# Optimization experiments

Measured on AMD Instinct MI355X. Metric: run time of the kernel, lower is better.

The kernel has to match this reference:

```python
import jax, jax.numpy as jnp
import numpy as np

DIM = 128; D_STATE = 16; D_CONV = 4; EXPAND = 2
D_INNER = DIM * EXPAND            # 256
DT_RANK = (DIM + 15) // 16        # 8
B, H, W = 2, 56, 56


def _ln(x, w, b):
    m = jnp.mean(x, -1, keepdims=True)
    v = jnp.var(x, -1, keepdims=True)
    return (x - m) * jax.lax.rsqrt(v + 1e-5) * w + b


def _mamba(x, in_w, conv_w, conv_b, xproj_w, dt_w, dt_b, A_log, Dp, out_w):
    # x: (B, L, DIM)
    Bb, L, _ = x.shape
    xz = x @ in_w.T                                   # (B,L,2*D_INNER)
    xi, z = jnp.split(xz, 2, axis=-1)
    # causal depthwise conv1d (pad left d_conv-1, truncate to L)
    xc = jnp.transpose(xi, (0, 2, 1))                 # (B,D_INNER,L)
    xc = jax.lax.conv_general_dilated(
        xc, conv_w, (1,), [(D_CONV - 1, 0)],
        dimension_numbers=('NCH', 'OIH', 'NCH'),
        feature_group_count=D_INNER) + conv_b[None, :, None]
    xs = jax.nn.silu(jnp.transpose(xc, (0, 2, 1)))    # (B,L,D_INNER)
    dbl = xs @ xproj_w.T                              # (B,L,DT_RANK+2*D_STATE)
    dt = jax.nn.softplus(dbl[..., :DT_RANK] @ dt_w.T + dt_b)   # (B,L,D_INNER)
    Bc = dbl[..., DT_RANK:DT_RANK + D_STATE]          # (B,L,D_STATE)
    Cc = dbl[..., DT_RANK + D_STATE:]                 # (B,L,D_STATE)
    A = -jnp.exp(A_log)                               # (D_INNER,D_STATE)
    dA = jnp.exp(dt[..., None] * A)                   # (B,L,D_INNER,D_STATE)
    dBu = (dt * xs)[..., None] * Bc[:, :, None, :]    # (B,L,D_INNER,D_STATE)

    def step(h, inp):
        a, bu, c = inp
        h = a * h + bu                                # (B,D_INNER,D_STATE)
        return h, jnp.einsum('bdn,bn->bd', h, c)

    h0 = jnp.zeros((Bb, D_INNER, D_STATE), x.dtype)
    _, ys = jax.lax.scan(step, h0, (jnp.moveaxis(dA, 1, 0),
                                    jnp.moveaxis(dBu, 1, 0),
                                    jnp.moveaxis(Cc, 1, 0)))
    y = jnp.moveaxis(ys, 0, 1) + xs * Dp              # (B,L,D_INNER)
    y = y * jax.nn.silu(z)
    return y @ out_w.T                                # (B,L,DIM)


def _forward(x, norm_h_w, norm_h_b, norm_v_w, norm_v_b,
             dw_w, dw_b, pw_w, pw_b,
             h_in_w, h_conv_w, h_conv_b, h_xproj_w, h_dt_w, h_dt_b, h_A_log, h_D, h_out_w,
             v_in_w, v_conv_w, v_conv_b, v_xproj_w, v_dt_w, v_dt_b, v_A_log, v_D, v_out_w,
             ca_fc1_w, ca_fc2_w):
    Bb, C, Hh, Ww = x.shape
    # local branch: depthwise 3x3 + GELU + 1x1
    lf = jax.lax.conv_general_dilated(
        x, dw_w, (1, 1), [(1, 1), (1, 1)],
        dimension_numbers=('NCHW', 'OIHW', 'NCHW'),
        feature_group_count=C) + dw_b[None, :, None, None]
    lf = jax.nn.gelu(lf, approximate=False)
    lf = jnp.einsum('bchw,oc->bohw', lf, pw_w[:, :, 0, 0]) + pw_b[None, :, None, None]
    # horizontal scan: row-major tokens
    xh = _ln(x.reshape(Bb, C, Hh * Ww).transpose(0, 2, 1), norm_h_w, norm_h_b)
    oh = _mamba(xh, h_in_w, h_conv_w, h_conv_b, h_xproj_w, h_dt_w, h_dt_b,
                h_A_log, h_D, h_out_w)
    oh = oh.transpose(0, 2, 1).reshape(Bb, C, Hh, Ww)
    # vertical scan: column-major tokens
    xv = _ln(jnp.transpose(x, (0, 1, 3, 2)).reshape(Bb, C, Ww * Hh).transpose(0, 2, 1),
             norm_v_w, norm_v_b)
    ov = _mamba(xv, v_in_w, v_conv_w, v_conv_b, v_xproj_w, v_dt_w, v_dt_b,
                v_A_log, v_D, v_out_w)
    ov = jnp.transpose(ov.transpose(0, 2, 1).reshape(Bb, C, Ww, Hh), (0, 1, 3, 2))
    fused = oh + ov + lf
    # channel attention
    y = jnp.mean(fused, axis=(2, 3))                  # (B,C)
    y = jax.nn.sigmoid(jax.nn.relu(y @ ca_fc1_w.T) @ ca_fc2_w.T)
    return fused * y[:, :, None, None] + x


def setup_inputs() -> dict:
    key = jax.random.key(0)
    ks = iter(jax.random.split(key, 64))
    def nrm(shape, scale):
        return jax.random.normal(next(ks), shape, jnp.float32) * scale
    d = {}
    d['x'] = nrm((B, DIM, H, W), 1.0)
    d['norm_h_w'] = jnp.ones((DIM,), jnp.float32); d['norm_h_b'] = jnp.zeros((DIM,), jnp.float32)
    d['norm_v_w'] = jnp.ones((DIM,), jnp.float32); d['norm_v_b'] = jnp.zeros((DIM,), jnp.float32)
    d['dw_w'] = nrm((DIM, 1, 3, 3), 1.0 / 3.0)
    d['dw_b'] = jnp.zeros((DIM,), jnp.float32)
    d['pw_w'] = nrm((DIM, DIM, 1, 1), DIM ** -0.5)
    d['pw_b'] = jnp.zeros((DIM,), jnp.float32)
    for p in ('h', 'v'):
        d[p + '_in_w'] = nrm((2 * D_INNER, DIM), DIM ** -0.5)
        d[p + '_conv_w'] = nrm((D_INNER, 1, D_CONV), D_CONV ** -0.5)
        d[p + '_conv_b'] = jnp.zeros((D_INNER,), jnp.float32)
        d[p + '_xproj_w'] = nrm((DT_RANK + 2 * D_STATE, D_INNER), D_INNER ** -0.5)
        d[p + '_dt_w'] = nrm((D_INNER, DT_RANK), DT_RANK ** -0.5)
        d[p + '_dt_b'] = jnp.full((D_INNER,), -2.0, jnp.float32)  # small positive dt
        d[p + '_A_log'] = jnp.log(jnp.tile(jnp.arange(1, D_STATE + 1, dtype=jnp.float32), (D_INNER, 1)))
        d[p + '_D'] = jnp.ones((D_INNER,), jnp.float32)
        d[p + '_out_w'] = nrm((DIM, D_INNER), D_INNER ** -0.5)
    d['ca_fc1_w'] = nrm((DIM // 4, DIM), DIM ** -0.5)
    d['ca_fc2_w'] = nrm((DIM, DIM // 4), (DIM // 4) ** -0.5)
    return d


def reference(x, norm_h_w, norm_h_b, norm_v_w, norm_v_b,
              dw_w, dw_b, pw_w, pw_b,
              h_in_w, h_conv_w, h_conv_b, h_xproj_w, h_dt_w, h_dt_b, h_A_log, h_D, h_out_w,
              v_in_w, v_conv_w, v_conv_b, v_xproj_w, v_dt_w, v_dt_b, v_A_log, v_D, v_out_w,
              ca_fc1_w, ca_fc2_w):
    return _forward(x, norm_h_w, norm_h_b, norm_v_w, norm_v_b,
                    dw_w, dw_b, pw_w, pw_b,
                    h_in_w, h_conv_w, h_conv_b, h_xproj_w, h_dt_w, h_dt_b, h_A_log, h_D, h_out_w,
                    v_in_w, v_conv_w, v_conv_b, v_xproj_w, v_dt_w, v_dt_b, v_A_log, v_D, v_out_w,
                    ca_fc1_w, ca_fc2_w)
```

## Files before the change

### kernel.cpp

```cpp
#include <hip/hip_runtime.h>
#include <hip/hip_bf16.h>

typedef __hip_bfloat16 bf16;
__device__ __forceinline__ float b2f(bf16 v){ return __bfloat162float(v); }
__device__ __forceinline__ bf16 f2b(float v){ return __float2bfloat16(v); }

typedef __attribute__((ext_vector_type(8))) short frag_ab;
typedef __attribute__((ext_vector_type(4))) float frag_cd;
typedef __attribute__((ext_vector_type(4))) short short4v;

__device__ __forceinline__ frag_ab ld_frag_2xb64(const bf16* p){
  union { frag_ab f; short4v h[2]; } u;
  u.h[0] = *reinterpret_cast<const short4v*>(p);
  u.h[1] = *reinterpret_cast<const short4v*>(p+4);
  return u.f;
}

#define LLEN 3136
#define BATCH 2
#define NCHUNK 49
#define LC 64

__global__ void k_front(const float* __restrict__ x, const float* __restrict__ dww,
                        const float* __restrict__ dwb, bf16* __restrict__ tmp,
                        const float* nhw_, const float* nhb_, const float* nvw_,
                        const float* nvb_, bf16* __restrict__ xln,
                        const float* __restrict__ h_inw, const float* __restrict__ v_inw,
                        const float* __restrict__ h_ow,  const float* __restrict__ v_ow,
                        const float* __restrict__ pww,   const float* __restrict__ h_xw,
                        const float* __restrict__ v_xw,
                        bf16* __restrict__ WBIN, bf16* __restrict__ WBOUT,
                        bf16* __restrict__ WBPW, bf16* __restrict__ WBX,
                        float* __restrict__ TSUMP){
  int blk = blockIdx.x;
  int tid = threadIdx.x;
  if (blk < 1024){
    int bc = blk & 255;
    int seg = blk >> 8;
    int c = bc & 127;
    const float* xp = x + (size_t)bc*LLEN;
    __shared__ float sxr[16][60];
    __shared__ float wsum[4];
    int r0 = seg*14;
    for (int idx = tid; idx < 16*56; idx += 256){
      int rr = idx/56, cc = idx%56;
      int gr = r0 - 1 + rr;
      sxr[rr][cc+1] = (gr >= 0 && gr < 56) ? xp[gr*56+cc] : 0.f;
    }
    if (tid < 16){ sxr[tid][0] = 0.f; sxr[tid][57] = 0.f; }
    float w[9];
    #pragma unroll
    for (int i=0;i<9;i++) w[i] = dww[c*9+i];
    float bias = dwb[c];
    __syncthreads();
    int pstart = seg * 784;
    float ts = 0.f;
    for (int p = pstart + tid; p < pstart + 784; p += 256){
      int i = p/56, j = p%56;
      int li = i - r0;
      float acc = bias;
      #pragma unroll
      for (int a=0;a<3;a++)
        #pragma unroll
        for (int bb=0;bb<3;bb++)
          acc += w[a*3+bb] * sxr[li+a][j+bb];
      float g = 0.5f*acc*(1.0f + erff(acc*0.70710678118654752f));
      bf16 gb = f2b(g);
      tmp[(size_t)bc*LLEN + p] = gb;
      ts += b2f(gb);
    }
    ts += __shfl_xor(ts, 1, 64);
    ts += __shfl_xor(ts, 2, 64);
    ts += __shfl_xor(ts, 4, 64);
    ts += __shfl_xor(ts, 8, 64);
    ts += __shfl_xor(ts, 16, 64);
    ts += __shfl_xor(ts, 32, 64);
    if ((tid & 63) == 0) wsum[tid >> 6] = ts;
    __syncthreads();
    if (tid == 0) TSUMP[seg*256 + bc] = wsum[0]+wsum[1]+wsum[2]+wsum[3];
  } else if (blk < 1136){
    int idx2 = blk - 1024;
    int h = idx2 % 56, b = idx2 / 56;
    __shared__ float sx[128][57];
    __shared__ float smean[56], srstd[56];
    __shared__ float wh[128], bh[128], wv_[128], bv_[128];
    if (tid < 128){ wh[tid]=nhw_[tid]; bh[tid]=nhb_[tid];
                    wv_[tid]=nvw_[tid]; bv_[tid]=nvb_[tid]; }
    for (int idx = tid; idx < 128*56; idx += 256){
      int c = idx / 56, w = idx % 56;
      sx[c][w] = x[((size_t)(b*128+c))*LLEN + h*56 + w];
    }
    __syncthreads();
    if (tid < 56){
      float s=0.f, s2=0.f;
      for (int c=0;c<128;c++){ float v = sx[c][tid]; s+=v; s2+=v*v; }
      float m = s*(1.f/128.f);
      float var = s2*(1.f/128.f) - m*m;
      smean[tid]=m; srstd[tid]=rsqrtf(var+1e-5f);
    }
    __syncthreads();
    bf16* outh = xln;
    bf16* outv = xln + (size_t)BATCH*LLEN*128;
    for (int idx = tid; idx < 56*128; idx += 256){
      int w = idx >> 7, c = idx & 127;
      float v = (sx[c][w]-smean[w])*srstd[w];
      outh[((size_t)b*LLEN + h*56 + w)*128 + c] = f2b(v*wh[c]+bh[c]);
      outv[((size_t)b*LLEN + w*56 + h)*128 + c] = f2b(v*wv_[c]+bv_[c]);
    }
  } else {
    int pblk = blk - 1136;
    int t16 = tid*16;
    if (pblk < 32){
      int g = pblk*4096 + t16;
      int dir = g >> 16, off = g & 65535;
      const float* src = (dir ? v_inw : h_inw) + off;
      bf16* dst = WBIN + g;
      #pragma unroll
      for (int r=0;r<4;r++){
        float4 w4 = *reinterpret_cast<const float4*>(src + r*4);
        bf16 t4[4] = {f2b(w4.x), f2b(w4.y), f2b(w4.z), f2b(w4.w)};
        *reinterpret_cast<double*>(dst + r*4) = *reinterpret_cast<double*>(t4);
      }
    } else if (pblk < 48){
      int g = (pblk-32)*4096 + t16;
      int dir = g >> 15, off = g & 32767;
      const float* src = (dir ? v_ow : h_ow) + off;
      bf16* dst = WBOUT + g;
      #pragma unroll
      for (int r=0;r<4;r++){
        float4 w4 = *reinterpret_cast<const float4*>(src + r*4);
        bf16 t4[4] = {f2b(w4.x), f2b(w4.y), f2b(w4.z), f2b(w4.w)};
        *reinterpret_cast<double*>(dst + r*4) = *reinterpret_cast<double*>(t4);
      }
    } else if (pblk < 52){
      int g = (pblk-48)*4096 + t16;
      const float* src = pww + g;
      bf16* dst = WBPW + g;
      #pragma unroll
      for (int r=0;r<4;r++){
        float4 w4 = *reinterpret_cast<const float4*>(src + r*4);
        bf16 t4[4] = {f2b(w4.x), f2b(w4.y), f2b(w4.z), f2b(w4.w)};
        *reinterpret_cast<double*>(dst + r*4) = *reinterpret_cast<double*>(t4);
      }
    } else if (pblk < 58){
      int g = (pblk-52)*4096 + t16;
      int dir = (g >= 12288) ? 1 : 0;
      int off = g - dir*12288;
      int rr = off >> 8, cc = off & 255;
      bf16* dst = WBX + g;
      if (rr < 40){
        const float* src = (dir ? v_xw : h_xw) + rr*256 + cc;
        #pragma unroll
        for (int r=0;r<4;r++){
          float4 w4 = *reinterpret_cast<const float4*>(src + r*4);
          bf16 t4[4] = {f2b(w4.x), f2b(w4.y), f2b(w4.z), f2b(w4.w)};
          *reinterpret_cast<double*>(dst + r*4) = *reinterpret_cast<double*>(t4);
        }
      } else {
        bf16 z4[4] = {f2b(0.f), f2b(0.f), f2b(0.f), f2b(0.f)};
        double zd = *reinterpret_cast<double*>(z4);
        #pragma unroll
        for (int r=0;r<4;r++) *reinterpret_cast<double*>(dst + r*4) = zd;
      }
    }
  }
}

__global__ void k_inproj(const bf16* __restrict__ xln, const bf16* __restrict__ WBIN,
                         bf16* __restrict__ XI, bf16* __restrict__ Z){
  int dir = blockIdx.z;
  const bf16* A = xln + (size_t)dir*BATCH*LLEN*128;
  const bf16* Wb = WBIN + (size_t)dir*512*128;
  int m0 = blockIdx.x*64;
  int npair = blockIdx.y*128;
  __shared__ __align__(16) bf16 sA[64][136];
  __shared__ __align__(16) bf16 sW[64][136];
  int tid = threadIdx.x;
  #pragma unroll
  for (int r=0;r<4;r++){
    int idx = tid + r*256;
    int row = idx >> 4, c8 = (idx & 15)*8;
    *reinterpret_cast<float4*>(&sA[row][c8]) =
        *reinterpret_cast<const float4*>(&A[(size_t)(m0+row)*128 + c8]);
  }
  int wv2 = tid >> 6, lane = tid & 63;
  int qd = lane >> 4, mr = lane & 15;
  bf16* dst = (npair < 256) ? XI : Z;
  int nbase0 = npair & 255;
  size_t dslab = (size_t)dir*BATCH*LLEN*256;
  #pragma unroll
  for (int nt=0; nt<2; nt++){
    int n0 = npair + nt*64;
    __syncthreads();
    #pragma unroll
    for (int r=0;r<4;r++){
      int idx = tid + r*256;
      int row = idx >> 4, c8 = (idx & 15)*8;
      *reinterpret_cast<float4*>(&sW[row][c8]) =
          *reinterpret_cast<const float4*>(&Wb[(size_t)(n0+row)*128 + c8]);
    }
    __syncthreads();
    frag_cd acc[4] = {};
    #pragma unroll
    for (int k0=0;k0<128;k0+=32){
      frag_ab af = *reinterpret_cast<frag_ab*>(&sA[wv2*16+mr][k0+qd*8]);
      #pragma unroll
      for (int t=0;t<4;t++){
        frag_ab bfr = *reinterpret_cast<frag_ab*>(&sW[t*16+mr][k0+qd*8]);
        acc[t] = __builtin_amdgcn_mfma_f32_16x16x32_bf16(af, bfr, acc[t], 0, 0, 0);
      }
    }
    int nb = nbase0 + nt*64;
    #pragma unroll
    for (int t=0;t<4;t++)
      #pragma unroll
      for (int r=0;r<4;r++){
        int row = m0 + wv2*16 + qd*4 + r;
        int col = nb + t*16 + mr;
        dst[dslab + (size_t)row*256 + col] = f2b(acc[t][r]);
      }
  }
}

__global__ void k_dbl(const bf16* __restrict__ XI,
                      const float* hcw, const float* hcb, const float* vcw, const float* vcb,
                      const bf16* __restrict__ WBX,
                      const float* hdw, const float* vdw, const float* hdb, const float* vdb,
                      bf16* __restrict__ XS2, bf16* __restrict__ DT2,
                      float* __restrict__ Bf, float* __restrict__ Cf){
  int m0 = blockIdx.x*64;
  int bd = m0 / LLEN;
  int l0m = m0 % LLEN;
  int dirq = bd >> 1;
  const bf16* XId = XI + (size_t)bd*LLEN*256;
  const bf16* Wb = WBX + (size_t)dirq*48*256;
  const float* cw = dirq ? vcw : hcw;
  const float* cb = dirq ? vcb : hcb;
  __shared__ __align__(16) bf16 sA[67][264];
  __shared__ __align__(16) bf16 sW[48][264];
  __shared__ float sdbl[64][49];
  int tid = threadIdx.x;
  for (int idx = tid; idx < 67*32; idx += 256){
    int row = idx >> 5, c8 = (idx & 31)*8;
    int l = l0m - 3 + row;
    float4 v = make_float4(0.f,0.f,0.f,0.f);
    if (l >= 0) v = *reinterpret_cast<const float4*>(&XId[(size_t)l*256 + c8]);
    *reinterpret_cast<float4*>(&sA[row][c8]) = v;
  }
  #pragma unroll
  for (int r=0;r<6;r++){
    int idx = tid + r*256;
    int row = idx >> 5, c8 = (idx & 31)*8;
    *reinterpret_cast<float4*>(&sW[row][c8]) =
        *reinterpret_cast<const float4*>(&Wb[(size_t)row*256 + c8]);
  }
  __syncthreads();
  {
    float w0=cw[tid*4], w1=cw[tid*4+1], w2=cw[tid*4+2], w3=cw[tid*4+3];
    float cbias = cb[tid];
    size_t x2base = ((size_t)bd*16 + (tid>>4))*LLEN + l0m;
    int c16 = tid & 15;
    float xm3 = b2f(sA[0][tid]), xm2 = b2f(sA[1][tid]), xm1 = b2f(sA[2][tid]);
    #pragma unroll 4
    for (int j=0;j<64;j++){
      float x0 = b2f(sA[j+3][tid]);
      float acc = cbias + w0*xm3 + w1*xm2 + w2*xm1 + w3*x0;
      float s = acc / (1.f + __expf(-acc));
      bf16 sv = f2b(s);
      sA[j][tid] = sv;
      XS2[(x2base + j)*16 + c16] = sv;
      xm3=xm2; xm2=xm1; xm1=x0;
    }
  }
  __syncthreads();
  int wv2 = tid >> 6, lane = tid & 63;
  int qd = lane >> 4, mr = lane & 15;
  frag_cd acc[3] = {};
  #pragma unroll
  for (int k0=0;k0<256;k0+=32){
    frag_ab af = *reinterpret_cast<frag_ab*>(&sA[wv2*16+mr][k0+qd*8]);
    #pragma unroll
    for (int t=0;t<3;t++){
      frag_ab bfr = *reinterpret_cast<frag_ab*>(&sW[t*16+mr][k0+qd*8]);
      acc[t] = __builtin_amdgcn_mfma_f32_16x16x32_bf16(af, bfr, acc[t], 0, 0, 0);
    }
  }
  #pragma unroll
  for (int t=0;t<3;t++)
    #pragma unroll
    for (int r=0;r<4;r++){
      int col = t*16 + mr;
      if (col < 40) sdbl[wv2*16 + qd*4 + r][col] = acc[t][r];
    }
  __syncthreads();
  const float* dtw = dirq ? vdw : hdw;
  const float* dtb = dirq ? vdb : hdb;
  float w8[8];
  #pragma unroll
  for (int r=0;r<8;r++) w8[r] = dtw[tid*8+r];
  float biasv = dtb[tid];
  size_t d2base = ((size_t)bd*16 + (tid>>4))*LLEN + l0m;
  int c16 = tid & 15;
  for (int row=0; row<64; row++){
    float a = biasv;
    #pragma unroll
    for (int r=0;r<8;r++) a += sdbl[row][r]*w8[r];
    float sv = (a > 20.f) ? a : __logf(1.f + __expf(a));
    DT2[(d2base + row)*16 + c16] = f2b(sv);
  }
  #pragma unroll
  for (int r=0;r<8;r++){
    int idx = tid + r*256;
    int row = idx >> 5, o = idx & 31;
    float v = sdbl[row][8+o];
    size_t rr = (size_t)(m0+row)*16;
    if (o < 16) Bf[rr + o] = v;
    else        Cf[rr + (o-16)] = v;
  }
}

__global__ void k_scan1(const bf16* __restrict__ DT2, const bf16* __restrict__ XS2,
                        const float* __restrict__ Bc, const float* hA, const float* vA,
                        float* __restrict__ Pbuf, float* __restrict__ Hbuf){
  int bd = blockIdx.z;
  int g  = blockIdx.y;
  int ck = blockIdx.x;
  int l0 = ck*LC;
  const float* Bd = Bc + (size_t)bd*LLEN*16;
  const float* Alog = (bd >> 1) ? vA : hA;
  int tid = threadIdx.x;
  int dl = tid >> 4, n = tid & 15;
  float A = -__expf(Alog[(g*16+dl)*16+n]);
  __shared__ float sdt[LC][16], sxs[LC][16], sB[LC][16];
  size_t base2 = (((size_t)bd*16 + g)*LLEN + l0)*16;
  #pragma unroll
  for (int r=0;r<4;r++){
    int idx = tid + r*256;
    sdt[idx>>4][idx&15] = b2f(DT2[base2 + idx]);
    sxs[idx>>4][idx&15] = b2f(XS2[base2 + idx]);
    (&sB[0][0])[idx] = Bd[(size_t)l0*16 + idx];
  }
  __syncthreads();
  float h = 0.f, P = 1.f;
  #pragma unroll 8
  for (int i=0;i<LC;i++){
    float a = sdt[i][dl];
    float u = sxs[i][dl];
    float dA = __expf(a * A);
    h = dA*h + (a*u)*sB[i][n];
    P *= dA;
  }
  size_t sidx = (((size_t)bd*16 + g)*NCHUNK + ck)*256 + tid;
  Pbuf[sidx] = P;
  Hbuf[sidx] = h;
}

__global__ void k_scan2(const float* __restrict__ Pbuf, float* __restrict__ Hbuf){
  int q = blockIdx.x;
  int tid = threadIdx.x;
  size_t qb = (size_t)q*NCHUNK*256 + tid;
  float Pv[7], Hv[7];
  float carry = 0.f;
  #pragma unroll
  for (int j=0;j<7;j++){
    Pv[j] = Pbuf[qb + (size_t)j*256];
    Hv[j] = Hbuf[qb + (size_t)j*256];
  }
  #pragma unroll
  for (int b=0;b<7;b++){
    float Pn[7], Hn[7];
    if (b < 6){
      #pragma unroll
      for (int j=0;j<7;j++){
        Pn[j] = Pbuf[qb + (size_t)((b+1)*7+j)*256];
        Hn[j] = Hbuf[qb + (size_t)((b+1)*7+j)*256];
      }
    }
    #pragma unroll
    for (int j=0;j<7;j++){
      Hbuf[qb + (size_t)(b*7+j)*256] = carry;
      carry = Pv[j]*carry + Hv[j];
    }
    if (b < 6){
      #pragma unroll
      for (int j=0;j<7;j++){ Pv[j] = Pn[j]; Hv[j] = Hn[j]; }
    }
  }
}

__global__ void k_scan3(const bf16* __restrict__ DT2, const bf16* __restrict__ XS2,
                        const float* __restrict__ Bc, const float* __restrict__ Cc,
                        const float* hA, const float* vA,
                        const float* __restrict__ Hbuf, bf16* __restrict__ ys){
  int bd = blockIdx.z;
  int g  = blockIdx.y;
  int ck = blockIdx.x;
  int l0 = ck*LC;
  const float* Bd = Bc + (size_t)bd*LLEN*16;
  const float* Cd = Cc + (size_t)bd*LLEN*16;
  bf16* yd = ys + (size_t)bd*LLEN*256;
  const float* Alog = (bd >> 1) ? vA : hA;
  int tid = threadIdx.x;
  int dl = tid >> 4, n = tid & 15;
  float A = -__expf(Alog[(g*16+dl)*16+n]);
  __shared__ float sdt[LC][16], sxs[LC][16], sB[LC][16], sC[LC][16];
  __shared__ float sp2[16][272];
  size_t base2 = (((size_t)bd*16 + g)*LLEN + l0)*16;
  #pragma unroll
  for (int r=0;r<4;r++){
    int idx = tid + r*256;
    sdt[idx>>4][idx&15] = b2f(DT2[base2 + idx]);
    sxs[idx>>4][idx&15] = b2f(XS2[base2 + idx]);
    (&sB[0][0])[idx] = Bd[(size_t)l0*16 + idx];
    (&sC[0][0])[idx] = Cd[(size_t)l0*16 + idx];
  }
  size_t sidx = (((size_t)bd*16 + g)*NCHUNK + ck)*256 + tid;
  float h = Hbuf[sidx];
  __syncthreads();
  int swz = dl*17 + n;
  int i_local = tid >> 4;
  int c16 = tid & 15;
  int rbase = c16*17;
  for (int i0=0; i0<LC; i0+=16){
    #pragma unroll
    for (int ii=0;ii<16;ii++){
      int i = i0 + ii;
      float a = sdt[i][dl];
      float u = sxs[i][dl];
      float dA = __expf(a * A);
      h = dA*h + (a*u)*sB[i][n];
      sp2[ii][swz] = h * sC[i][n];
    }
    __syncthreads();
    const float* row = &sp2[i_local][rbase];
    float s = 0.f;
    #pragma unroll
    for (int k=0;k<16;k++) s += row[k];
    yd[(size_t)(l0+i0+i_local)*256 + g*16 + c16] = f2b(s);
    __syncthreads();
  }
}

__global__ void k_outgemm(const bf16* __restrict__ ys, const bf16* __restrict__ XS2,
                          const bf16* __restrict__ Z, const float* __restrict__ hD,
                          const float* __restrict__ vD, const bf16* __restrict__ WBOUT,
                          bf16* __restrict__ OD, float* __restrict__ OSUMP){
  int dir = blockIdx.y;
  size_t slab = (size_t)dir*BATCH*LLEN*256;
  const bf16* Wb = WBOUT + (size_t)dir*128*256;
  const float* Dw = dir ? vD : hD;
  bf16* od = OD + (size_t)dir*BATCH*LLEN*128;
  int m0 = blockIdx.x*32;
  int bd = dir*2 + m0/LLEN;
  int lbase = m0 % LLEN;
  __shared__ __align__(16) bf16 sA[32][264];
  __shared__ __align__(16) bf16 sW[64][264];
  __shared__ float scol[128];
  int tid = threadIdx.x;
  if (tid < 128) scol[tid] = 0.f;
  #pragma unroll
  for (int r=0;r<4;r++){
    int idx = tid + r*256;
    int row = idx >> 5, c8 = (idx & 31)*8;
    size_t e = slab + (size_t)(m0+row)*256 + c8;
    size_t e2 = (((size_t)bd*16 + (c8>>4))*LLEN + lbase + row)*16 + (c8&15);
    bf16 yb[8], xb[8], zb[8], ob[8];
    *reinterpret_cast<float4*>(yb) = *reinterpret_cast<const float4*>(&ys[e]);
    *reinterpret_cast<float4*>(xb) = *reinterpret_cast<const float4*>(&XS2[e2]);
    *reinterpret_cast<float4*>(zb) = *reinterpret_cast<const float4*>(&Z[e]);
    #pragma unroll
    for (int j=0;j<8;j++){
      float Dv = Dw[c8 + j];
      float yv = b2f(yb[j]) + b2f(xb[j])*Dv;
      float zv = b2f(zb[j]);
      ob[j] = f2b(yv * (zv/(1.f+__expf(-zv))));
    }
    *reinterpret_cast<float4*>(&sA[row][c8]) = *reinterpret_cast<float4*>(ob);
  }
  int wv2 = tid >> 6, lane = tid & 63;
  int qd = lane >> 4, mr = lane & 15;
  int msub = wv2 & 1, tpair = (wv2 >> 1)*2;
  #pragma unroll
  for (int nh=0; nh<2; nh++){
    int n0 = nh*64;
    __syncthreads();
    #pragma unroll
    for (int r=0;r<8;r++){
      int idx = tid + r*256;
      int row = idx >> 5, c8 = (idx & 31)*8;
      *reinterpret_cast<float4*>(&sW[row][c8]) =
          *reinterpret_cast<const float4*>(&Wb[(size_t)(n0+row)*256 + c8]);
    }
    __syncthreads();
    frag_cd acc[2] = {};
    #pragma unroll
    for (int k0=0;k0<256;k0+=32){
      frag_ab af = *reinterpret_cast<frag_ab*>(&sA[msub*16+mr][k0+qd*8]);
      #pragma unroll
      for (int i=0;i<2;i++){
        frag_ab bfr = *reinterpret_cast<frag_ab*>(&sW[(tpair+i)*16+mr][k0+qd*8]);
        acc[i] = __builtin_amdgcn_mfma_f32_16x16x32_bf16(af, bfr, acc[i], 0, 0, 0);
      }
    }
    #pragma unroll
    for (int i=0;i<2;i++){
      float cs = 0.f;
      #pragma unroll
      for (int r=0;r<4;r++){
        int row = m0 + msub*16 + qd*4 + r;
        int col = n0 + (tpair+i)*16 + mr;
        bf16 ov = f2b(acc[i][r]);
        od[(size_t)row*128 + col] = ov;
        cs += b2f(ov);
      }
      cs += __shfl_xor(cs, 16, 64);
      cs += __shfl_xor(cs, 32, 64);
      if (qd == 0) atomicAdd(&scol[n0 + (tpair+i)*16 + mr], cs);
    }
  }
  __syncthreads();
  if (tid < 128){
    int b = m0 / LLEN;
    int t = blockIdx.x % 98;
    OSUMP[(((size_t)(dir*2 + b)*98) + t)*128 + tid] = scol[tid];
  }
}

__global__ void k_gate(const float* __restrict__ TSUMP, const float* __restrict__ OSUMP,
                       const bf16* __restrict__ WBPW, const float* __restrict__ pwb,
                       const float* __restrict__ fc1, const float* __restrict__ fc2,
                       float* __restrict__ GATE){
  int b = blockIdx.x;
  int tid = threadIdx.x;
  __shared__ float tsh[128], ym[128], s1g[32];
  if (tid < 128)
    tsh[tid] = TSUMP[0*256 + b*128 + tid] + TSUMP[1*256 + b*128 + tid]
             + TSUMP[2*256 + b*128 + tid] + TSUMP[3*256 + b*128 + tid];
  __syncthreads();
  if (tid < 128){
    float os = 0.f;
    for (int dir=0; dir<2; dir++)
      for (int t=0; t<98; t++)
        os += OSUMP[(((size_t)(dir*2 + b)*98) + t)*128 + tid];
    float pwpart = 0.f;
    #pragma unroll 8
    for (int c=0; c<128; c++)
      pwpart += b2f(WBPW[tid*128 + c]) * tsh[c];
    ym[tid] = (pwpart + os)*(1.f/(float)LLEN) + pwb[tid];
  }
  __syncthreads();
  {
    int o = tid >> 3, part = tid & 7;
    float a = 0.f;
    #pragma unroll
    for (int k=0;k<16;k++) a += ym[part*16 + k] * fc1[o*128 + part*16 + k];
    a += __shfl_xor(a, 1, 8);
    a += __shfl_xor(a, 2, 8);
    a += __shfl_xor(a, 4, 8);
    if (part == 0) s1g[o] = fmaxf(a, 0.f);
  }
  __syncthreads();
  if (tid < 128){
    float a = 0.f;
    #pragma unroll
    for (int j=0;j<32;j++) a += s1g[j]*fc2[tid*32+j];
    GATE[b*128+tid] = 1.f/(1.f+__expf(-a));
  }
}

__global__ void k_pwcomb(const bf16* __restrict__ tmp, const bf16* __restrict__ WBPW,
                         const float* __restrict__ pwb, const bf16* __restrict__ OD,
                         const float* __restrict__ x, float* __restrict__ out,
                         const float* __restrict__ GATE){
  int p0 = blockIdx.x * 64;
  int m0 = blockIdx.y * 64;
  int b  = blockIdx.z;
  const bf16* T = tmp + (size_t)b*128*LLEN;
  const bf16* od0 = OD + (size_t)b*LLEN*128;
  const bf16* od1 = OD + (size_t)(BATCH + b)*LLEN*128;
  __shared__ __align__(16) bf16 sA[64][136];
  __shared__ __align__(16) bf16 sBt[64][132];
  __shared__ float sOD[64][65];
  int tid = threadIdx.x;
  #pragma unroll
  for (int r=0;r<4;r++){
    int idx = tid + r*256;
    int row = idx >> 4, c8 = (idx & 15)*8;
    *reinterpret_cast<float4*>(&sA[row][c8]) =
        *reinterpret_cast<const float4*>(&WBPW[(size_t)(m0+row)*128 + c8]);
  }
  #pragma unroll
  for (int r=0;r<8;r++){
    int idx = tid + r*256;
    int c = idx >> 4, p4 = (idx & 15)*4;
    union { double d; bf16 v[4]; } u;
    u.d = *reinterpret_cast<const double*>(&T[(size_t)c*LLEN + p0 + p4]);
    #pragma unroll
    for (int j=0;j<4;j++) sBt[p4+j][c] = u.v[j];
  }
  #pragma unroll
  for (int r=0;r<8;r++){
    int idx = tid + r*256;
    int prow = idx >> 5, mp = (idx & 31)*2;
    int p = p0 + prow;
    int pi = p/56, pj = p%56;
    int pt = pj*56 + pi;
    bf16 a0[2], a1[2];
    *reinterpret_cast<float*>(a0) = *reinterpret_cast<const float*>(&od0[(size_t)p*128 + m0 + mp]);
    *reinterpret_cast<float*>(a1) = *reinterpret_cast<const float*>(&od1[(size_t)pt*128 + m0 + mp]);
    sOD[prow][mp]   = b2f(a0[0]) + b2f(a1[0]);
    sOD[prow][mp+1] = b2f(a0[1]) + b2f(a1[1]);
  }
  __syncthreads();
  int wv2 = tid >> 6, lane = tid & 63;
  int qd = lane >> 4, mr = lane & 15;
  frag_cd acc[4] = {};
  #pragma unroll
  for (int k0=0;k0<128;k0+=32){
    frag_ab af = *reinterpret_cast<frag_ab*>(&sA[wv2*16+mr][k0+qd*8]);
    #pragma unroll
    for (int t=0;t<4;t++){
      frag_ab bfr = ld_frag_2xb64(&sBt[t*16+mr][k0+qd*8]);
      acc[t] = __builtin_amdgcn_mfma_f32_16x16x32_bf16(af, bfr, acc[t], 0, 0, 0);
    }
  }
  #pragma unroll
  for (int r=0;r<4;r++){
    int m = m0 + wv2*16 + qd*4 + r;
    float bias = pwb[m];
    float g = GATE[b*128 + m];
    #pragma unroll
    for (int t=0;t<4;t++){
      float val = acc[t][r] + bias + sOD[t*16+mr][m - m0];
      int p = p0 + t*16 + mr;
      size_t i = ((size_t)b*128 + m)*LLEN + p;
      out[i] = val*g + x[i];
    }
  }
}

extern "C" void kernel_launch(void* const* d_in, const int* in_sizes, int n_in,
                              void* d_out, int out_size, void* d_ws, size_t ws_size,
                              hipStream_t stream) {
  const float* x      = (const float*)d_in[0];
  const float* nhw    = (const float*)d_in[1];
  const float* nhb    = (const float*)d_in[2];
  const float* nvw    = (const float*)d_in[3];
  const float* nvb    = (const float*)d_in[4];
  const float* dww    = (const float*)d_in[5];
  const float* dwb    = (const float*)d_in[6];
  const float* pww    = (const float*)d_in[7];
  const float* pwb    = (const float*)d_in[8];
  const float* h_inw  = (const float*)d_in[9];
  const float* h_cw   = (const float*)d_in[10];
  const float* h_cb   = (const float*)d_in[11];
  const float* h_xw   = (const float*)d_in[12];
  const float* h_dtw  = (const float*)d_in[13];
  const float* h_dtb  = (const float*)d_in[14];
  const float* h_Al   = (const float*)d_in[15];
  const float* h_D    = (const float*)d_in[16];
  const float* h_ow   = (const float*)d_in[17];
  const float* v_inw  = (const float*)d_in[18];
  const float* v_cw   = (const float*)d_in[19];
  const float* v_cb   = (const float*)d_in[20];
  const float* v_xw   = (const float*)d_in[21];
  const float* v_dtw  = (const float*)d_in[22];
  const float* v_dtb  = (const float*)d_in[23];
  const float* v_Al   = (const float*)d_in[24];
  const float* v_D    = (const float*)d_in[25];
  const float* v_ow   = (const float*)d_in[26];
  const float* fc1    = (const float*)d_in[27];
  const float* fc2    = (const float*)d_in[28];

  float* out = (float*)d_out;

  bf16*  WBIN  = (bf16*) ((char*)d_out + 0);
  bf16*  WBOUT = (bf16*) ((char*)d_out + 262144);
  bf16*  WBX   = (bf16*) ((char*)d_out + 393216);
  float* TSUMP = (float*)((char*)d_out + 442368);
  float* OSUMP = (float*)((char*)d_out + 446464);

  char* base = (char*)d_ws;
  bf16*  XLN   = (bf16*)(base + 1605632);
  bf16*  DT2   = (bf16*)(base + 0);
  bf16*  OD    = (bf16*)(base + 0);
  bf16*  XI    = (bf16*)(base + 6422528);
  bf16*  YS    = (bf16*)(base + 6422528);
  bf16*  Z     = (bf16*)(base + 12845056);
  bf16*  XS2   = (bf16*)(base + 19267584);
  float* Bf    = (float*)(base + 25690112);
  float* Cf    = (float*)(base + 26492928);
  float* Hbuf  = (float*)(base + 27295744);
  bf16*  TMP   = (bf16*)(base + 30508032);
  float* Pbuf  = (float*)(base + 32113664);
  bf16*  WBPW  = (bf16*) (base + 35326464);
  float* GATE  = (float*)(base + 35359232);

  k_front<<<dim3(1024 + 56*BATCH + 64), dim3(256), 0, stream>>>(
      x, dww, dwb, TMP, nhw, nhb, nvw, nvb, XLN,
      h_inw, v_inw, h_ow, v_ow, pww, h_xw, v_xw, WBIN, WBOUT, WBPW, WBX, TSUMP);
  k_inproj<<<dim3(98,4,2), dim3(256), 0, stream>>>(XLN, WBIN, XI, Z);
  k_dbl<<<dim3(196), dim3(256), 0, stream>>>(XI, h_cw, h_cb, v_cw, v_cb,
                                             WBX, h_dtw, v_dtw, h_dtb, v_dtb,
                                             XS2, DT2, Bf, Cf);
  k_scan1<<<dim3(NCHUNK,16,4), dim3(256), 0, stream>>>(DT2, XS2, Bf, h_Al, v_Al, Pbuf, Hbuf);
  k_scan2<<<dim3(64), dim3(256), 0, stream>>>(Pbuf, Hbuf);
  k_scan3<<<dim3(NCHUNK,16,4), dim3(256), 0, stream>>>(DT2, XS2, Bf, Cf, h_Al, v_Al, Hbuf, YS);
  k_outgemm<<<dim3(196,2), dim3(256), 0, stream>>>(YS, XS2, Z, h_D, v_D, WBOUT, OD, OSUMP);
  k_gate<<<dim3(BATCH), dim3(256), 0, stream>>>(TSUMP, OSUMP, WBPW, pwb, fc1, fc2, GATE);
  k_pwcomb<<<dim3(49,2,BATCH), dim3(256), 0, stream>>>(TMP, WBPW, pwb, OD, x, out, GATE);
}
```

Before: 215.8 us.

## Fold chunk-carry scan into scan3 and halve k_dbl row tile

Removes the separate k_scan2 launch. Each k_scan3 block now recomputes its incoming chunk state by serially combining all preceding chunks' (P,H) pairs from global memory, which trades one kernel launch and a dependency for redundant work of up to 48 steps per block. Separately, k_dbl now processes 32 rows per block instead of 64 and launches twice as many blocks for more parallelism. In the GEMM phase only two of the four waves do MFMA work.

```diff
diff --git a/kernel.cpp b/kernel.cpp
--- a/kernel.cpp
+++ b/kernel.cpp
@@ -228,7 +228,7 @@
                       const float* hdw, const float* vdw, const float* hdb, const float* vdb,
                       bf16* __restrict__ XS2, bf16* __restrict__ DT2,
                       float* __restrict__ Bf, float* __restrict__ Cf){
-  int m0 = blockIdx.x*64;
+  int m0 = blockIdx.x*32;
   int bd = m0 / LLEN;
   int l0m = m0 % LLEN;
   int dirq = bd >> 1;
@@ -236,11 +236,11 @@
   const bf16* Wb = WBX + (size_t)dirq*48*256;
   const float* cw = dirq ? vcw : hcw;
   const float* cb = dirq ? vcb : hcb;
-  __shared__ __align__(16) bf16 sA[67][264];
+  __shared__ __align__(16) bf16 sA[35][264];
   __shared__ __align__(16) bf16 sW[48][264];
-  __shared__ float sdbl[64][49];
-  int tid = threadIdx.x;
-  for (int idx = tid; idx < 67*32; idx += 256){
+  __shared__ float sdbl[32][49];
+  int tid = threadIdx.x;
+  for (int idx = tid; idx < 35*32; idx += 256){
     int row = idx >> 5, c8 = (idx & 31)*8;
     int l = l0m - 3 + row;
     float4 v = make_float4(0.f,0.f,0.f,0.f);
@@ -262,7 +262,7 @@
     int c16 = tid & 15;
     float xm3 = b2f(sA[0][tid]), xm2 = b2f(sA[1][tid]), xm1 = b2f(sA[2][tid]);
     #pragma unroll 4
-    for (int j=0;j<64;j++){
+    for (int j=0;j<32;j++){
       float x0 = b2f(sA[j+3][tid]);
       float acc = cbias + w0*xm3 + w1*xm2 + w2*xm1 + w3*x0;
       float s = acc / (1.f + __expf(-acc));
@@ -275,23 +275,25 @@
   __syncthreads();
   int wv2 = tid >> 6, lane = tid & 63;
   int qd = lane >> 4, mr = lane & 15;
-  frag_cd acc[3] = {};
-  #pragma unroll
-  for (int k0=0;k0<256;k0+=32){
-    frag_ab af = *reinterpret_cast<frag_ab*>(&sA[wv2*16+mr][k0+qd*8]);
-    #pragma unroll
-    for (int t=0;t<3;t++){
-      frag_ab bfr = *reinterpret_cast<frag_ab*>(&sW[t*16+mr][k0+qd*8]);
-      acc[t] = __builtin_amdgcn_mfma_f32_16x16x32_bf16(af, bfr, acc[t], 0, 0, 0);
-    }
-  }
-  #pragma unroll
-  for (int t=0;t<3;t++)
-    #pragma unroll
-    for (int r=0;r<4;r++){
-      int col = t*16 + mr;
-      if (col < 40) sdbl[wv2*16 + qd*4 + r][col] = acc[t][r];
-    }
+  if (wv2 < 2){
+    frag_cd acc[3] = {};
+    #pragma unroll
+    for (int k0=0;k0<256;k0+=32){
+      frag_ab af = *reinterpret_cast<frag_ab*>(&sA[wv2*16+mr][k0+qd*8]);
+      #pragma unroll
+      for (int t=0;t<3;t++){
+        frag_ab bfr = *reinterpret_cast<frag_ab*>(&sW[t*16+mr][k0+qd*8]);
+        acc[t] = __builtin_amdgcn_mfma_f32_16x16x32_bf16(af, bfr, acc[t], 0, 0, 0);
+      }
+    }
+    #pragma unroll
+    for (int t=0;t<3;t++)
+      #pragma unroll
+      for (int r=0;r<4;r++){
+        int col = t*16 + mr;
+        if (col < 40) sdbl[wv2*16 + qd*4 + r][col] = acc[t][r];
+      }
+  }
   __syncthreads();
   const float* dtw = dirq ? vdw : hdw;
   const float* dtb = dirq ? vdb : hdb;
@@ -301,7 +303,7 @@
   float biasv = dtb[tid];
   size_t d2base = ((size_t)bd*16 + (tid>>4))*LLEN + l0m;
   int c16 = tid & 15;
-  for (int row=0; row<64; row++){
+  for (int row=0; row<32; row++){
     float a = biasv;
     #pragma unroll
     for (int r=0;r<8;r++) a += sdbl[row][r]*w8[r];
@@ -309,7 +311,7 @@
     DT2[(d2base + row)*16 + c16] = f2b(sv);
   }
   #pragma unroll
-  for (int r=0;r<8;r++){
+  for (int r=0;r<4;r++){
     int idx = tid + r*256;
     int row = idx >> 5, o = idx & 31;
     float v = sdbl[row][8+o];
@@ -355,43 +357,11 @@
   Hbuf[sidx] = h;
 }
 
-__global__ void k_scan2(const float* __restrict__ Pbuf, float* __restrict__ Hbuf){
-  int q = blockIdx.x;
-  int tid = threadIdx.x;
-  size_t qb = (size_t)q*NCHUNK*256 + tid;
-  float Pv[7], Hv[7];
-  float carry = 0.f;
-  #pragma unroll
-  for (int j=0;j<7;j++){
-    Pv[j] = Pbuf[qb + (size_t)j*256];
-    Hv[j] = Hbuf[qb + (size_t)j*256];
-  }
-  #pragma unroll
-  for (int b=0;b<7;b++){
-    float Pn[7], Hn[7];
-    if (b < 6){
-      #pragma unroll
-      for (int j=0;j<7;j++){
-        Pn[j] = Pbuf[qb + (size_t)((b+1)*7+j)*256];
-        Hn[j] = Hbuf[qb + (size_t)((b+1)*7+j)*256];
-      }
-    }
-    #pragma unroll
-    for (int j=0;j<7;j++){
-      Hbuf[qb + (size_t)(b*7+j)*256] = carry;
-      carry = Pv[j]*carry + Hv[j];
-    }
-    if (b < 6){
-      #pragma unroll
-      for (int j=0;j<7;j++){ Pv[j] = Pn[j]; Hv[j] = Hn[j]; }
-    }
-  }
-}
-
 __global__ void k_scan3(const bf16* __restrict__ DT2, const bf16* __restrict__ XS2,
                         const float* __restrict__ Bc, const float* __restrict__ Cc,
                         const float* hA, const float* vA,
-                        const float* __restrict__ Hbuf, bf16* __restrict__ ys){
+                        const float* __restrict__ Pbuf, const float* __restrict__ Hbuf,
+                        bf16* __restrict__ ys){
   int bd = blockIdx.z;
   int g  = blockIdx.y;
   int ck = blockIdx.x;
@@ -414,8 +384,23 @@
     (&sB[0][0])[idx] = Bd[(size_t)l0*16 + idx];
     (&sC[0][0])[idx] = Cd[(size_t)l0*16 + idx];
   }
-  size_t sidx = (((size_t)bd*16 + g)*NCHUNK + ck)*256 + tid;
-  float h = Hbuf[sidx];
+  float h = 0.f;
+  {
+    size_t qbase = (size_t)(bd*16 + g)*NCHUNK*256 + tid;
+    int k = 0;
+    for (; k+8 <= ck; k += 8){
+      float Pv[8], Hv[8];
+      #pragma unroll
+      for (int j=0;j<8;j++){
+        Pv[j] = Pbuf[qbase + (size_t)(k+j)*256];
+        Hv[j] = Hbuf[qbase + (size_t)(k+j)*256];
+      }
+      #pragma unroll
+      for (int j=0;j<8;j++) h = Pv[j]*h + Hv[j];
+    }
+    for (; k < ck; ++k)
+      h = Pbuf[qbase + (size_t)k*256]*h + Hbuf[qbase + (size_t)k*256];
+  }
   __syncthreads();
   int swz = dl*17 + n;
   int i_local = tid >> 4;
@@ -700,12 +685,12 @@
       x, dww, dwb, TMP, nhw, nhb, nvw, nvb, XLN,
       h_inw, v_inw, h_ow, v_ow, pww, h_xw, v_xw, WBIN, WBOUT, WBPW, WBX, TSUMP);
   k_inproj<<<dim3(98,4,2), dim3(256), 0, stream>>>(XLN, WBIN, XI, Z);
-  k_dbl<<<dim3(196), dim3(256), 0, stream>>>(XI, h_cw, h_cb, v_cw, v_cb,
+  k_dbl<<<dim3(392), dim3(256), 0, stream>>>(XI, h_cw, h_cb, v_cw, v_cb,
                                              WBX, h_dtw, v_dtw, h_dtb, v_dtb,
                                              XS2, DT2, Bf, Cf);
   k_scan1<<<dim3(NCHUNK,16,4), dim3(256), 0, stream>>>(DT2, XS2, Bf, h_Al, v_Al, Pbuf, Hbuf);
-  k_scan2<<<dim3(64), dim3(256), 0, stream>>>(Pbuf, Hbuf);
-  k_scan3<<<dim3(NCHUNK,16,4), dim3(256), 0, stream>>>(DT2, XS2, Bf, Cf, h_Al, v_Al, Hbuf, YS);
+  k_scan3<<<dim3(NCHUNK,16,4), dim3(256), 0, stream>>>(DT2, XS2, Bf, Cf, h_Al, v_Al,
+                                                       Pbuf, Hbuf, YS);
   k_outgemm<<<dim3(196,2), dim3(256), 0, stream>>>(YS, XS2, Z, h_D, v_D, WBOUT, OD, OSUMP);
   k_gate<<<dim3(BATCH), dim3(256), 0, stream>>>(TSUMP, OSUMP, WBPW, pwb, fc1, fc2, GATE);
   k_pwcomb<<<dim3(49,2,BATCH), dim3(256), 0, stream>>>(TMP, WBPW, pwb, OD, x, out, GATE);
```

After: 211.4 us. 2.1% less time.
